# Kernel optimization log

Hardware: AMD Instinct MI355X
Metric: run time of the kernel (lower is better)

The kernel has to match this reference:

```python
import jax, jax.numpy as jnp
import numpy as np

N, L, E, NB, H = 128, 200, 128, 2, 2
ITEM = 50000
TEMP = 0.2
HD = E // H


def _ln(x, g, b, eps=1e-8):
    m = x.mean(-1, keepdims=True)
    v = ((x - m) ** 2).mean(-1, keepdims=True)
    return (x - m) / jnp.sqrt(v + eps) * g + b


def setup_inputs() -> dict:
    key = jax.random.key(0)
    ks = jax.random.split(key, 20)
    rng = np.random.default_rng(0)
    log_seqs = rng.integers(1, ITEM + 1, size=(N, L))
    lens = rng.integers(20, L + 1, size=(N,))
    log_seqs[np.arange(L)[None, :] < (L - lens[:, None])] = 0  # left padding, id 0
    pos_seqs = rng.integers(1, ITEM + 1, size=(N, L))
    neg_seqs = rng.integers(1, ITEM + 1, size=(N, L))
    item_emb = jax.random.normal(ks[0], (ITEM + 1, E), jnp.float32) * 0.02
    item_emb = item_emb.at[0].set(0.0)  # padding_idx=0
    s = 1.0 / np.sqrt(E)
    return {
        "item_emb": item_emb,
        "pos_emb": jax.random.normal(ks[1], (L + 1, E), jnp.float32) * 0.02,
        "W_asp": jax.random.normal(ks[2], (16, E, E), jnp.float32) * s,
        "w_weight": jax.random.normal(ks[3], (2 * E,), jnp.float32) * (1.0 / np.sqrt(2 * E)),
        "w_bias": jnp.zeros((), jnp.float32),
        "attn_ln_g": jnp.ones((NB, E), jnp.float32),
        "attn_ln_b": jnp.zeros((NB, E), jnp.float32),
        "in_proj_w": jax.random.normal(ks[4], (NB, 3 * E, E), jnp.float32) * s,
        "in_proj_b": jnp.zeros((NB, 3 * E), jnp.float32),
        "out_proj_w": jax.random.normal(ks[5], (NB, E, E), jnp.float32) * s,
        "out_proj_b": jnp.zeros((NB, E), jnp.float32),
        "fwd_ln_g": jnp.ones((NB, E), jnp.float32),
        "fwd_ln_b": jnp.zeros((NB, E), jnp.float32),
        "conv1_w": jax.random.normal(ks[6], (NB, E, E), jnp.float32) * s,
        "conv1_b": jnp.zeros((NB, E), jnp.float32),
        "conv2_w": jax.random.normal(ks[7], (NB, E, E), jnp.float32) * s,
        "conv2_b": jnp.zeros((NB, E), jnp.float32),
        "last_ln_g": jnp.ones((E,), jnp.float32),
        "last_ln_b": jnp.zeros((E,), jnp.float32),
        "user_ids": jnp.asarray(rng.integers(0, 100000, size=(N,)), jnp.int32),
        "log_seqs": jnp.asarray(log_seqs, jnp.int32),
        "pos_seqs": jnp.asarray(pos_seqs, jnp.int32),
        "neg_seqs": jnp.asarray(neg_seqs, jnp.int32),
        "epoch": 1,
    }


def reference(item_emb, pos_emb, W_asp, w_weight, w_bias, attn_ln_g, attn_ln_b,
              in_proj_w, in_proj_b, out_proj_w, out_proj_b, fwd_ln_g, fwd_ln_b,
              conv1_w, conv1_b, conv2_w, conv2_b, last_ln_g, last_ln_b,
              user_ids, log_seqs, pos_seqs, neg_seqs, epoch):
    tmask = (log_seqs == 0)                               # (N,L) True=pad
    validL = (~tmask).astype(item_emb.dtype)              # (N,L)
    seqs0 = item_emb[log_seqs] * validL[..., None]
    pos_embs = item_emb[pos_seqs] * validL[..., None]
    neg_embs = item_emb[neg_seqs] * validL[..., None]

    validE = jnp.concatenate([validL, validL[:, -1:]], 1)  # (N,L+1)
    kv_save = jnp.concatenate([seqs0, pos_embs[:, -1:, :]], 1)  # (N,L+1,E)

    def aspects(x, valid, residual):
        a = jnp.einsum('nli,aoi->nlao', x, W_asp)          # 16 expert GEMMs batched
        if residual:
            a = a + x[:, :, None, :]
            a = a / (jnp.linalg.norm(a, axis=-1, keepdims=True) + 1e-8)
        return a * valid[:, :, None, None]

    kv4 = aspects(kv_save, validE, True)                   # (N,L+1,16,E)
    temp = aspects(kv_save, validE, False)
    nvalid = validE.sum()
    cent_loss = jnp.linalg.norm(kv_save * validE[..., None] - temp.mean(2), axis=-1).sum() / nvalid

    norm_x = kv4 / (jnp.linalg.norm(kv4, axis=-1, keepdims=True) + 1e-8)
    pos_s = (norm_x * norm_x).sum(-1)                      # (N,L+1,16)
    ttl = jnp.einsum('nlae,nlbe->nlab', norm_x, norm_x)    # pairwise cosine sims
    mi = -(pos_s / TEMP - jnp.log(jnp.exp(ttl / TEMP).sum(-1)))
    ind_loss = (mi * validE[:, :, None]).sum() / nvalid

    s = kv4.sum(2)                                         # (N,L+1,E)
    q = jnp.cumsum(s, 1) - s                               # exclusive cumsum
    cnt = jnp.cumsum(validE, 1) - validE
    q = q / (16.0 * cnt + 1e-8)[..., None] * validE[..., None]

    w_q, w_a = w_weight[:E], w_weight[E:]

    def gate(qv, a4):                                      # learned softmax gating
        logits = (qv @ w_q)[:, :, None] + a4 @ w_a + w_bias
        w = jax.nn.softmax(logits, axis=2)
        return (a4 * w[..., None]).sum(2)

    re_all = gate(q, kv4)                                  # (N,L+1,E)
    re_emb = re_all[:, :L] + kv4[:, :L].mean(2)

    neg_kv4 = aspects(neg_embs, validL, True)
    q2 = q[:, 1:, :] * validL[..., None]
    neg_t = gate(q2, neg_kv4) + neg_kv4.mean(2)
    pos_t = re_all[:, 1:, :] * validL[..., None] + (kv4[:, 1:] * validL[..., None, None]).mean(2)

    seqs = re_emb * (E ** 0.5) + pos_emb[jnp.arange(L)][None]
    seqs = seqs * validL[..., None]
    causal = jnp.where(jnp.tril(jnp.ones((L, L), bool)), 0.0, -1e9)
    scale = HD ** -0.5
    for i in range(NB):
        Qn = _ln(seqs, attn_ln_g[i], attn_ln_b[i])
        qp = Qn @ in_proj_w[i][:E].T + in_proj_b[i][:E]
        kp = seqs @ in_proj_w[i][E:2 * E].T + in_proj_b[i][E:2 * E]
        vp = seqs @ in_proj_w[i][2 * E:].T + in_proj_b[i][2 * E:]
        sp = lambda x: x.reshape(N, L, H, HD).transpose(0, 2, 1, 3)
        att = jax.nn.softmax(jnp.einsum('nhqd,nhkd->nhqk', sp(qp), sp(kp)) * scale + causal, axis=-1)
        o = jnp.einsum('nhqk,nhkd->nhqd', att, sp(vp)).transpose(0, 2, 1, 3).reshape(N, L, E)
        seqs = Qn + (o @ out_proj_w[i].T + out_proj_b[i])
        seqs = _ln(seqs, fwd_ln_g[i], fwd_ln_b[i])
        h = jax.nn.relu(seqs @ conv1_w[i].T + conv1_b[i])
        seqs = (h @ conv2_w[i].T + conv2_b[i]) + seqs
        seqs = seqs * validL[..., None]
    log_feats = _ln(seqs, last_ln_g, last_ln_b)
    pos_logits = (log_feats * pos_t).sum(-1)
    neg_logits = (log_feats * neg_t).sum(-1)
    return (pos_logits, neg_logits, ind_loss, cent_loss)
```

## Files before the change

### kernel.cpp

```cpp
#include <hip/hip_runtime.h>
#include <hip/hip_bf16.h>
#include <cstddef>

typedef __attribute__((ext_vector_type(8))) short bf16x8;
typedef __attribute__((ext_vector_type(4))) float f32x4;
typedef unsigned short ushort_t;

__device__ __forceinline__ short f2bf(float f) {
    __hip_bfloat16 h = __float2bfloat16(f);
    return __builtin_bit_cast(short, h);
}
__device__ __forceinline__ float bf2f(short s) {
    unsigned u = ((unsigned)(unsigned short)s) << 16;
    return __builtin_bit_cast(float, u);
}
__device__ __forceinline__ unsigned pk2(float a, float b) {
    return (unsigned)(unsigned short)f2bf(a) | ((unsigned)(unsigned short)f2bf(b) << 16);
}

__global__ void cvt_all(const float* __restrict__ s0, const float* __restrict__ s1,
                        const float* __restrict__ s2, const float* __restrict__ s3,
                        const float* __restrict__ s4, ushort_t* __restrict__ dst) {
    const int i = blockIdx.x * 256 + threadIdx.x;
    const int mat = i >> 14;
    const int wm = i & 16383;
    const int blk = wm >> 9;
    const int t = blk >> 2, f = blk & 3;
    const int lane = (wm >> 3) & 63;
    const int j = wm & 7;
    const int g4 = lane >> 4, nn = lane & 15;
    const int o = t * 16 + nn;
    const int k = f * 32 + g4 * 8 + j;
    const int srcoff = o * 128 + k;
    const float* src; int mbase;
    if (mat < 16)      { src = s0; mbase = mat; }
    else if (mat < 22) { src = s1; mbase = mat - 16; }
    else if (mat < 24) { src = s2; mbase = mat - 22; }
    else if (mat < 26) { src = s3; mbase = mat - 24; }
    else               { src = s4; mbase = mat - 26; }
    float v = src[(size_t)mbase * 16384 + srcoff];
    if (mat < 16 && o == k) v += 1.f;
    dst[i] = (ushort_t)f2bf(v);
}

__global__ __launch_bounds__(512, 1) void aspects2_kernel(
        const float* __restrict__ item_emb,
        const int* __restrict__ log_seqs, const int* __restrict__ pos_seqs,
        const int* __restrict__ neg_seqs,
        const ushort_t* __restrict__ Wab,
        const float* __restrict__ w_weight,
        const float* __restrict__ pos_emb,
        float* __restrict__ Gout, float* __restrict__ seqs,
        float* __restrict__ validE, float* __restrict__ validL,
        float* __restrict__ pInd, float* __restrict__ pCent,
        int nLossBlocks) {
    __shared__ ushort_t rsb[32 * 2184];
    __shared__ ushort_t xsb[32 * 136];
    __shared__ ushort_t wal_b[128];
    __shared__ int sidx[32];
    __shared__ float s_red[512];
    __shared__ float s_lg[512];
    __shared__ float s_pos[512];
    __shared__ float vld[32];
    __shared__ float centw[32];
    __shared__ float miw[32];

    const int tid = threadIdx.x;
    const int row0 = blockIdx.x * 32;
    const bool losses = (int)blockIdx.x < nLossBlocks;
    const int lane = tid & 63, w = tid >> 6;
    const int g4 = lane >> 4, nn = lane & 15;

    if (tid < 32) {
        const int rg = row0 + tid;
        int si; float vl;
        if (rg < 25728) {
            const int nq = rg / 201, l = rg % 201;
            if (l < 200) { si = log_seqs[nq * 200 + l]; vl = (si != 0) ? 1.f : 0.f; }
            else { vl = (log_seqs[nq * 200 + 199] != 0) ? 1.f : 0.f; si = pos_seqs[nq * 200 + 199]; }
            validE[rg] = vl;
        } else {
            const int rr = rg - 25728;
            vl = (log_seqs[rr] != 0) ? 1.f : 0.f;
            si = neg_seqs[rr];
            validL[rr] = vl;
        }
        sidx[tid] = si;
        vld[tid] = vl;
    }
    if (tid < 128) wal_b[tid] = (ushort_t)f2bf(w_weight[128 + tid]);
    __syncthreads();

    {
        const int r = tid >> 4, c8 = (tid & 15) * 8;
        const float vl = vld[r];
        const float* px = &item_emb[(size_t)sidx[r] * 128 + c8];
        const float4 a = *(const float4*)px;
        const float4 b = *(const float4*)(px + 4);
        *(int2*)&xsb[r * 136 + c8] = make_int2(
            (int)pk2(a.x * vl, a.y * vl), (int)pk2(a.z * vl, a.w * vl));
        *(int2*)&xsb[r * 136 + c8 + 4] = make_int2(
            (int)pk2(b.x * vl, b.y * vl), (int)pk2(b.z * vl, b.w * vl));
    }
    __syncthreads();

    bf16x8 xf0[4], xf1[4], waf[4];
#pragma unroll
    for (int f = 0; f < 4; ++f) {
        xf0[f] = *(const bf16x8*)&xsb[nn * 136 + f * 32 + g4 * 8];
        xf1[f] = *(const bf16x8*)&xsb[(nn + 16) * 136 + f * 32 + g4 * 8];
        waf[f] = *(const bf16x8*)&wal_b[f * 32 + g4 * 8];
    }

    for (int al = 0; al < 2; ++al) {
        const int a = w * 2 + al;
        const ushort_t* wbase = Wab + (size_t)a * 16384 + lane * 8;
#pragma unroll
        for (int t = 0; t < 8; ++t) {
            f32x4 d0 = {0.f, 0.f, 0.f, 0.f}, d1 = d0;
#pragma unroll
            for (int f = 0; f < 4; ++f) {
                bf16x8 wf = *(const bf16x8*)&wbase[(t * 4 + f) * 512];
                d0 = __builtin_amdgcn_mfma_f32_16x16x32_bf16(wf, xf0[f], d0, 0, 0, 0);
                d1 = __builtin_amdgcn_mfma_f32_16x16x32_bf16(wf, xf1[f], d1, 0, 0, 0);
            }
            const int o0 = t * 16 + g4 * 4;
            *(int2*)&rsb[nn * 2184 + a * 136 + o0] = make_int2(
                (int)pk2(d0[0], d0[1]), (int)pk2(d0[2], d0[3]));
            *(int2*)&rsb[(nn + 16) * 2184 + a * 136 + o0] = make_int2(
                (int)pk2(d1[0], d1[1]), (int)pk2(d1[2], d1[3]));
        }
    }
    __syncthreads();

    f32x4 gram0 = {0.f,0.f,0.f,0.f}, gram1 = gram0, gram2 = gram0, gram3 = gram0;
#pragma unroll
    for (int rl = 0; rl < 4; ++rl) {
        const int row = w * 4 + rl;
        f32x4 dgr = {0.f, 0.f, 0.f, 0.f}, dlp = dgr;
#pragma unroll
        for (int f = 0; f < 4; ++f) {
            bf16x8 fr = *(const bf16x8*)&rsb[row * 2184 + nn * 136 + f * 32 + g4 * 8];
            dgr = __builtin_amdgcn_mfma_f32_16x16x32_bf16(fr, fr, dgr, 0, 0, 0);
            dlp = __builtin_amdgcn_mfma_f32_16x16x32_bf16(fr, waf[f], dlp, 0, 0, 0);
        }
        if (rl == 0) gram0 = dgr; else if (rl == 1) gram1 = dgr;
        else if (rl == 2) gram2 = dgr; else gram3 = dgr;
        if (g4 == (nn >> 2)) s_red[row * 16 + nn] = dgr[nn & 3];
        if (nn == 0) {
#pragma unroll
            for (int r = 0; r < 4; ++r) s_lg[row * 16 + g4 * 4 + r] = dlp[r];
        }
    }
    __syncthreads();

    {
        const float nrm = sqrtf(s_red[tid]);
        const float inv1 = 1.f / (nrm + 1e-8f);
        const float n2 = nrm * inv1;
        const float sg = inv1 / (n2 + 1e-8f);
        const float ts = n2 / (n2 + 1e-8f);
        const float logit = s_lg[tid] * inv1;
        float mx = logit;
#pragma unroll
        for (int m = 1; m < 16; m <<= 1) mx = fmaxf(mx, __shfl_xor(mx, m, 16));
        const float e = __expf(logit - mx);
        float ssum = e;
#pragma unroll
        for (int m = 1; m < 16; m <<= 1) ssum += __shfl_xor(ssum, m, 16);
        s_red[tid] = sg;
        s_pos[tid] = ts * ts * 5.f;
        s_lg[tid] = (e / ssum + 0.0625f) * inv1;
    }
    __syncthreads();

    {
        const int row = tid >> 4, ol = tid & 15, o8 = ol * 8;
        float g[8] = {0.f, 0.f, 0.f, 0.f, 0.f, 0.f, 0.f, 0.f};
        float sr[8] = {0.f, 0.f, 0.f, 0.f, 0.f, 0.f, 0.f, 0.f};
#pragma unroll
        for (int a = 0; a < 16; ++a) {
            const bf16x8 vb = *(const bf16x8*)&rsb[row * 2184 + a * 136 + o8];
            const float gw = s_lg[row * 16 + a];
#pragma unroll
            for (int j = 0; j < 8; ++j) {
                const float v = bf2f(vb[j]);
                g[j] += v * gw;
                if (losses) sr[j] += v;
            }
        }
        float* go = &Gout[(size_t)(row0 + row) * 128 + o8];
        *(float4*)go       = make_float4(g[0], g[1], g[2], g[3]);
        *(float4*)(go + 4) = make_float4(g[4], g[5], g[6], g[7]);
        if (losses) {
            const int rg = row0 + row;
            const int nq = rg / 201, l = rg % 201;
            if (l < 200) {
                const float4 p0 = *(const float4*)&pos_emb[l * 128 + o8];
                const float4 p1 = *(const float4*)&pos_emb[l * 128 + o8 + 4];
                const float vv = vld[row];
                float* so = &seqs[(size_t)(nq * 200 + l) * 128 + o8];
                const float SQ = 11.313708498984761f;
                *(float4*)so = make_float4((g[0] * SQ + p0.x) * vv, (g[1] * SQ + p0.y) * vv,
                                           (g[2] * SQ + p0.z) * vv, (g[3] * SQ + p0.w) * vv);
                *(float4*)(so + 4) = make_float4((g[4] * SQ + p1.x) * vv, (g[5] * SQ + p1.y) * vv,
                                                 (g[6] * SQ + p1.z) * vv, (g[7] * SQ + p1.w) * vv);
            }
            const bf16x8 xb = *(const bf16x8*)&xsb[row * 136 + o8];
            float c = 0.f;
#pragma unroll
            for (int j = 0; j < 8; ++j) {
                const float dd = 2.f * bf2f(xb[j]) - sr[j] * 0.0625f;
                c += dd * dd;
            }
            c += __shfl_xor(c, 1, 64);
            c += __shfl_xor(c, 2, 64);
            c += __shfl_xor(c, 4, 64);
            c += __shfl_xor(c, 8, 64);
            if (ol == 0) centw[row] = sqrtf(c) * vld[row];
        }
    }

    if (losses) {
#pragma unroll
        for (int rl = 0; rl < 4; ++rl) {
            const int row = w * 4 + rl;
            const f32x4 dd = (rl == 0) ? gram0 : (rl == 1) ? gram1 : (rl == 2) ? gram2 : gram3;
            const float sgb = s_red[row * 16 + nn];
            float mis = 0.f;
#pragma unroll
            for (int r = 0; r < 4; ++r) {
                const int a = g4 * 4 + r;
                const float sga = s_red[row * 16 + a];
                float eb = __expf(5.f * dd[r] * sga * sgb);
#pragma unroll
                for (int m = 1; m < 16; m <<= 1) eb += __shfl_xor(eb, m, 16);
                mis += -(s_pos[row * 16 + a] - logf(eb));
            }
            mis += __shfl_xor(mis, 16, 64);
            mis += __shfl_xor(mis, 32, 64);
            if (lane == 0) miw[row] = mis * vld[row];
        }
        __syncthreads();
        if (tid == 0) {
            float si = 0.f, sc = 0.f;
#pragma unroll
            for (int r = 0; r < 32; ++r) { si += miw[r]; sc += centw[r]; }
            pInd[blockIdx.x] = si;
            pCent[blockIdx.x] = sc;
        }
    }
}

__global__ __launch_bounds__(64) void qkv_kernel(const float* __restrict__ X,
                                                 const ushort_t* __restrict__ W3,
                                                 const float* __restrict__ b3,
                                                 const float* __restrict__ lng,
                                                 const float* __restrict__ lnb,
                                                 float* __restrict__ Xn,
                                                 ushort_t* __restrict__ qo,
                                                 ushort_t* __restrict__ ko,
                                                 ushort_t* __restrict__ vo) {
    const int lane = threadIdx.x & 63;
    const int q = lane >> 4, nn = lane & 15;
    const int m0 = blockIdx.x * 16;
    float xv[4][8];
    float s = 0.f, sq = 0.f;
    const float* xr = &X[(size_t)(m0 + nn) * 128];
#pragma unroll
    for (int f = 0; f < 4; ++f) {
        const float4 a = *(const float4*)&xr[f * 32 + q * 8];
        const float4 b = *(const float4*)&xr[f * 32 + q * 8 + 4];
        xv[f][0] = a.x; xv[f][1] = a.y; xv[f][2] = a.z; xv[f][3] = a.w;
        xv[f][4] = b.x; xv[f][5] = b.y; xv[f][6] = b.z; xv[f][7] = b.w;
        s += (a.x + a.y) + (a.z + a.w) + (b.x + b.y) + (b.z + b.w);
        sq += (a.x * a.x + a.y * a.y) + (a.z * a.z + a.w * a.w)
            + (b.x * b.x + b.y * b.y) + (b.z * b.z + b.w * b.w);
    }
    bf16x8 afr[4];
#pragma unroll
    for (int f = 0; f < 4; ++f) {
        bf16x8 v;
#pragma unroll
        for (int j = 0; j < 8; ++j) v[j] = f2bf(xv[f][j]);
        afr[f] = v;
    }
    s += __shfl_xor(s, 16, 64);  s += __shfl_xor(s, 32, 64);
    sq += __shfl_xor(sq, 16, 64); sq += __shfl_xor(sq, 32, 64);
    const float mean = s * 0.0078125f;
    const float var = fmaxf(sq * 0.0078125f - mean * mean, 0.f);
    const float inv = rsqrtf(var + 1e-8f);
    bf16x8 afq[4];
#pragma unroll
    for (int f = 0; f < 4; ++f) {
        const int c0 = f * 32 + q * 8;
        const float4 ga = *(const float4*)&lng[c0];
        const float4 gb = *(const float4*)&lng[c0 + 4];
        const float4 ba = *(const float4*)&lnb[c0];
        const float4 bb = *(const float4*)&lnb[c0 + 4];
        float y[8];
        y[0] = (xv[f][0] - mean) * inv * ga.x + ba.x;
        y[1] = (xv[f][1] - mean) * inv * ga.y + ba.y;
        y[2] = (xv[f][2] - mean) * inv * ga.z + ba.z;
        y[3] = (xv[f][3] - mean) * inv * ga.w + ba.w;
        y[4] = (xv[f][4] - mean) * inv * gb.x + bb.x;
        y[5] = (xv[f][5] - mean) * inv * gb.y + bb.y;
        y[6] = (xv[f][6] - mean) * inv * gb.z + bb.z;
        y[7] = (xv[f][7] - mean) * inv * gb.w + bb.w;
        float* xo = &Xn[(size_t)(m0 + nn) * 128 + c0];
        *(float4*)xo       = make_float4(y[0], y[1], y[2], y[3]);
        *(float4*)(xo + 4) = make_float4(y[4], y[5], y[6], y[7]);
        bf16x8 v;
#pragma unroll
        for (int j = 0; j < 8; ++j) v[j] = f2bf(y[j]);
        afq[f] = v;
    }
    ushort_t* const outs[3] = {qo, ko, vo};
#pragma unroll
    for (int mi = 0; mi < 3; ++mi) {
        const ushort_t* wbase = W3 + (size_t)mi * 16384 + lane * 8;
        f32x4 acc[8];
#pragma unroll
        for (int t = 0; t < 8; ++t) acc[t] = (f32x4){0.f, 0.f, 0.f, 0.f};
#pragma unroll
        for (int t = 0; t < 8; ++t) {
#pragma unroll
            for (int f = 0; f < 4; ++f) {
                bf16x8 b = *(const bf16x8*)&wbase[(t * 4 + f) * 512];
                acc[t] = __builtin_amdgcn_mfma_f32_16x16x32_bf16(
                    (mi == 0) ? afq[f] : afr[f], b, acc[t], 0, 0, 0);
            }
        }
        const float* bi = b3 + mi * 128;
        ushort_t* outp = outs[mi];
#pragma unroll
        for (int t = 0; t < 8; ++t) {
            const int n = t * 16 + nn;
            const float bv = bi[n];
#pragma unroll
            for (int r = 0; r < 4; ++r) {
                const int row = m0 + q * 4 + r;
                outp[(size_t)row * 128 + n] = (ushort_t)f2bf(acc[t][r] + bv);
            }
        }
    }
}

template <int LAST>
__global__ __launch_bounds__(64) void ffn_kernel(const ushort_t* __restrict__ attno,
                                                 const ushort_t* __restrict__ outWb,
                                                 const float* __restrict__ outB,
                                                 const float* __restrict__ resQn,
                                                 const float* __restrict__ lng,
                                                 const float* __restrict__ lnb,
                                                 const ushort_t* __restrict__ c1wb,
                                                 const float* __restrict__ c1b,
                                                 const ushort_t* __restrict__ c2wb,
                                                 const float* __restrict__ c2b,
                                                 const float* __restrict__ validL,
                                                 float* __restrict__ seqs,
                                                 const float* __restrict__ lastg,
                                                 const float* __restrict__ lastb,
                                                 const float* __restrict__ G,
                                                 const float* __restrict__ negt,
                                                 float* __restrict__ outp) {
    __shared__ ushort_t hls[16 * 136];
    const int lane = threadIdx.x & 63;
    const int q = lane >> 4, nn = lane & 15;
    const int m0 = blockIdx.x * 16;

    bf16x8 af[4];
    {
        const ushort_t* xb = &attno[(size_t)(m0 + nn) * 128];
#pragma unroll
        for (int f = 0; f < 4; ++f) af[f] = *(const bf16x8*)&xb[f * 32 + q * 8];
    }
    f32x4 acc[8];
#pragma unroll
    for (int t = 0; t < 8; ++t) acc[t] = (f32x4){0.f, 0.f, 0.f, 0.f};
    {
        const ushort_t* wbase = outWb + lane * 8;
#pragma unroll
        for (int t = 0; t < 8; ++t)
#pragma unroll
            for (int f = 0; f < 4; ++f) {
                bf16x8 b = *(const bf16x8*)&wbase[(t * 4 + f) * 512];
                acc[t] = __builtin_amdgcn_mfma_f32_16x16x32_bf16(af[f], b, acc[t], 0, 0, 0);
            }
    }
    float y[8][4];
    float s[4] = {0.f, 0.f, 0.f, 0.f}, sq[4] = {0.f, 0.f, 0.f, 0.f};
#pragma unroll
    for (int t = 0; t < 8; ++t) {
        const int n = t * 16 + nn;
        const float bi = outB[n];
#pragma unroll
        for (int r = 0; r < 4; ++r) {
            const float v = acc[t][r] + bi + resQn[(size_t)(m0 + q * 4 + r) * 128 + n];
            y[t][r] = v;
            s[r] += v;
            sq[r] += v * v;
        }
    }
#pragma unroll
    for (int m = 1; m < 16; m <<= 1) {
#pragma unroll
        for (int r = 0; r < 4; ++r) {
            s[r] += __shfl_xor(s[r], m, 64);
            sq[r] += __shfl_xor(sq[r], m, 64);
        }
    }
#pragma unroll
    for (int r = 0; r < 4; ++r) {
        const float mean = s[r] * 0.0078125f;
        const float var = fmaxf(sq[r] * 0.0078125f - mean * mean, 0.f);
        const float inv = rsqrtf(var + 1e-8f);
        s[r] = mean; sq[r] = inv;
    }
#pragma unroll
    for (int t = 0; t < 8; ++t) {
        const int n = t * 16 + nn;
        const float g = lng[n], b = lnb[n];
#pragma unroll
        for (int r = 0; r < 4; ++r) {
            const float v = (y[t][r] - s[r]) * sq[r] * g + b;
            y[t][r] = v;
            hls[(q * 4 + r) * 136 + n] = (ushort_t)f2bf(v);
        }
    }
    __syncthreads();
    {
        const ushort_t* xb = &hls[nn * 136];
#pragma unroll
        for (int f = 0; f < 4; ++f) af[f] = *(const bf16x8*)&xb[f * 32 + q * 8];
    }
    f32x4 acc2[8];
#pragma unroll
    for (int t = 0; t < 8; ++t) acc2[t] = (f32x4){0.f, 0.f, 0.f, 0.f};
    {
        const ushort_t* wbase = c1wb + lane * 8;
#pragma unroll
        for (int t = 0; t < 8; ++t)
#pragma unroll
            for (int f = 0; f < 4; ++f) {
                bf16x8 b = *(const bf16x8*)&wbase[(t * 4 + f) * 512];
                acc2[t] = __builtin_amdgcn_mfma_f32_16x16x32_bf16(af[f], b, acc2[t], 0, 0, 0);
            }
    }
    __syncthreads();
#pragma unroll
    for (int t = 0; t < 8; ++t) {
        const int n = t * 16 + nn;
        const float bi = c1b[n];
#pragma unroll
        for (int r = 0; r < 4; ++r)
            hls[(q * 4 + r) * 136 + n] = (ushort_t)f2bf(fmaxf(acc2[t][r] + bi, 0.f));
    }
    __syncthreads();
    {
        const ushort_t* xb = &hls[nn * 136];
#pragma unroll
        for (int f = 0; f < 4; ++f) af[f] = *(const bf16x8*)&xb[f * 32 + q * 8];
    }
    f32x4 acc3[8];
#pragma unroll
    for (int t = 0; t < 8; ++t) acc3[t] = (f32x4){0.f, 0.f, 0.f, 0.f};
    {
        const ushort_t* wbase = c2wb + lane * 8;
#pragma unroll
        for (int t = 0; t < 8; ++t)
#pragma unroll
            for (int f = 0; f < 4; ++f) {
                bf16x8 b = *(const bf16x8*)&wbase[(t * 4 + f) * 512];
                acc3[t] = __builtin_amdgcn_mfma_f32_16x16x32_bf16(af[f], b, acc3[t], 0, 0, 0);
            }
    }
    float mk[4];
#pragma unroll
    for (int r = 0; r < 4; ++r) mk[r] = validL[m0 + q * 4 + r];

    if constexpr (!LAST) {
#pragma unroll
        for (int t = 0; t < 8; ++t) {
            const int n = t * 16 + nn;
            const float bi = c2b[n];
#pragma unroll
            for (int r = 0; r < 4; ++r) {
                const int row = m0 + q * 4 + r;
                seqs[(size_t)row * 128 + n] = (acc3[t][r] + bi + y[t][r]) * mk[r];
            }
        }
    } else {
        float ov[8][4];
        float s2[4] = {0.f, 0.f, 0.f, 0.f}, q2[4] = {0.f, 0.f, 0.f, 0.f};
#pragma unroll
        for (int t = 0; t < 8; ++t) {
            const int n = t * 16 + nn;
            const float bi = c2b[n];
#pragma unroll
            for (int r = 0; r < 4; ++r) {
                const float v = (acc3[t][r] + bi + y[t][r]) * mk[r];
                ov[t][r] = v;
                s2[r] += v;
                q2[r] += v * v;
            }
        }
#pragma unroll
        for (int m = 1; m < 16; m <<= 1) {
#pragma unroll
            for (int r = 0; r < 4; ++r) {
                s2[r] += __shfl_xor(s2[r], m, 64);
                q2[r] += __shfl_xor(q2[r], m, 64);
            }
        }
#pragma unroll
        for (int r = 0; r < 4; ++r) {
            const float mean = s2[r] * 0.0078125f;
            const float var = fmaxf(q2[r] * 0.0078125f - mean * mean, 0.f);
            const float inv = rsqrtf(var + 1e-8f);
            s2[r] = mean; q2[r] = inv;
        }
        float sp[4] = {0.f, 0.f, 0.f, 0.f}, sn[4] = {0.f, 0.f, 0.f, 0.f};
        int nqr[4], lr[4];
#pragma unroll
        for (int r = 0; r < 4; ++r) {
            const int row = m0 + q * 4 + r;
            nqr[r] = row / 200;
            lr[r] = row - nqr[r] * 200;
        }
#pragma unroll
        for (int t = 0; t < 8; ++t) {
            const int n = t * 16 + nn;
            const float g = lastg[n], b = lastb[n];
#pragma unroll
            for (int r = 0; r < 4; ++r) {
                const int row = m0 + q * 4 + r;
                const float yln = (ov[t][r] - s2[r]) * q2[r] * g + b;
                sp[r] += yln * G[((size_t)nqr[r] * 201 + lr[r] + 1) * 128 + n];
                sn[r] += yln * negt[(size_t)row * 128 + n];
            }
        }
#pragma unroll
        for (int m = 1; m < 16; m <<= 1) {
#pragma unroll
            for (int r = 0; r < 4; ++r) {
                sp[r] += __shfl_xor(sp[r], m, 64);
                sn[r] += __shfl_xor(sn[r], m, 64);
            }
        }
        if (nn == 0) {
#pragma unroll
            for (int r = 0; r < 4; ++r) {
                const int row = m0 + q * 4 + r;
                outp[row] = sp[r] * mk[r];
                outp[25600 + row] = sn[r];
            }
        }
    }
}

__global__ void reduce_kernel(const float* __restrict__ pInd, const float* __restrict__ pCent,
                              int nblk, const float* __restrict__ validE, int nve,
                              float* __restrict__ outp) {
    __shared__ float a1[256], a2[256], a3[256];
    const int tid = threadIdx.x;
    float si = 0.f, sc = 0.f, nv = 0.f;
    for (int t = tid; t < nblk; t += 256) { si += pInd[t]; sc += pCent[t]; }
    for (int t = tid; t < nve; t += 256) nv += validE[t];
    a1[tid] = si; a2[tid] = sc; a3[tid] = nv;
    __syncthreads();
    for (int s = 128; s > 0; s >>= 1) {
        if (tid < s) { a1[tid] += a1[tid + s]; a2[tid] += a2[tid + s]; a3[tid] += a3[tid + s]; }
        __syncthreads();
    }
    if (tid == 0) { outp[0] = a1[0] / a3[0]; outp[1] = a2[0] / a3[0]; }
}

__global__ __launch_bounds__(256) void attn_kernel(const ushort_t* __restrict__ qp,
                                                   const ushort_t* __restrict__ kp,
                                                   const ushort_t* __restrict__ vp,
                                                   ushort_t* __restrict__ outp) {
    __shared__ ushort_t KsU[2048];
    __shared__ ushort_t VtU[2560];
    __shared__ ushort_t Pb[2560];

    const int tid = threadIdx.x, lane = tid & 63, w = tid >> 6;
    const int b = blockIdx.x;
    const int nh = b >> 2, qt = b & 3;
    const int n = nh >> 1, h = nh & 1;
    const size_t base = (size_t)n * 200 * 128 + (size_t)h * 64;
    const int qw = qt * 64 + w * 16;
    const bool wactive = qw < 200;
    const int q15 = lane & 15, g4 = lane >> 4;
    const int qglob = qw + q15;

    bf16x8 qf[2];
    {
        const int qr = (qglob < 200) ? qglob : 199;
#pragma unroll
        for (int f = 0; f < 2; ++f)
            qf[f] = *(const bf16x8*)&qp[base + (size_t)qr * 128 + f * 32 + g4 * 8];
    }
    f32x4 Oacc[4];
#pragma unroll
    for (int nt = 0; nt < 4; ++nt) Oacc[nt] = (f32x4){0.f, 0.f, 0.f, 0.f};
    float mrun = -1e30f, lrun = 0.f;

    const int kmax = min(200, qt * 64 + 64);
    ushort_t* PbW = Pb + w * 640;

    for (int jt = 0; jt < kmax; jt += 32) {
        __syncthreads();
        {
            const int k = tid >> 3, e0 = (tid & 7) * 8;
            const int krow = jt + k;
            int4 a = make_int4(0, 0, 0, 0);
            if (krow < 200) a = *(const int4*)&kp[base + (size_t)krow * 128 + e0];
            *(int4*)&KsU[(k * 128 + ((e0 * 2) ^ ((k & 7) << 4))) >> 1] = a;
        }
        {
            const int k = tid & 31, e0 = (tid >> 5) * 8;
            const int vrow = jt + k;
            int4 a = make_int4(0, 0, 0, 0);
            if (vrow < 200) a = *(const int4*)&vp[base + (size_t)vrow * 128 + e0];
            VtU[(e0 + 0) * 40 + k] = (ushort_t)((unsigned)a.x & 0xFFFF);
            VtU[(e0 + 1) * 40 + k] = (ushort_t)((unsigned)a.x >> 16);
            VtU[(e0 + 2) * 40 + k] = (ushort_t)((unsigned)a.y & 0xFFFF);
            VtU[(e0 + 3) * 40 + k] = (ushort_t)((unsigned)a.y >> 16);
            VtU[(e0 + 4) * 40 + k] = (ushort_t)((unsigned)a.z & 0xFFFF);
            VtU[(e0 + 5) * 40 + k] = (ushort_t)((unsigned)a.z >> 16);
            VtU[(e0 + 6) * 40 + k] = (ushort_t)((unsigned)a.w & 0xFFFF);
            VtU[(e0 + 7) * 40 + k] = (ushort_t)((unsigned)a.w >> 16);
        }
        __syncthreads();
        if (!wactive) continue;

        f32x4 d0 = {0.f, 0.f, 0.f, 0.f}, d1 = d0;
#pragma unroll
        for (int f = 0; f < 2; ++f) {
            const int ebyte = g4 * 16 + f * 64;
            const int sw = ebyte ^ ((q15 & 7) << 4);
            bf16x8 a0 = *(const bf16x8*)&KsU[(q15 * 128 + sw) >> 1];
            bf16x8 a1 = *(const bf16x8*)&KsU[((q15 + 16) * 128 + sw) >> 1];
            d0 = __builtin_amdgcn_mfma_f32_16x16x32_bf16(a0, qf[f], d0, 0, 0, 0);
            d1 = __builtin_amdgcn_mfma_f32_16x16x32_bf16(a1, qf[f], d1, 0, 0, 0);
        }
        const int kb = jt + g4 * 4;
        float p[8];
        float tmax = -1e30f;
#pragma unroll
        for (int r = 0; r < 4; ++r) {
            const float s0 = (kb + r      <= qglob) ? d0[r] * 0.125f : -1e30f;
            const float s1 = (kb + r + 16 <= qglob) ? d1[r] * 0.125f : -1e30f;
            p[r] = s0; p[r + 4] = s1;
            tmax = fmaxf(tmax, fmaxf(s0, s1));
        }
        tmax = fmaxf(tmax, __shfl_xor(tmax, 16, 64));
        tmax = fmaxf(tmax, __shfl_xor(tmax, 32, 64));
        const float mnew = fmaxf(mrun, tmax);
        const float corr = __expf(mrun - mnew);
        mrun = mnew;
        float tsum = 0.f;
#pragma unroll
        for (int i = 0; i < 8; ++i) {
            float pe = __expf(p[i] - mnew);
            pe = bf2f(f2bf(pe));
            p[i] = pe;
            tsum += pe;
        }
        tsum += __shfl_xor(tsum, 16, 64);
        tsum += __shfl_xor(tsum, 32, 64);
        lrun = lrun * corr + tsum;
        const int kl = g4 * 4;
        *(unsigned*)&PbW[q15 * 40 + kl]          = pk2(p[0], p[1]);
        *(unsigned*)&PbW[q15 * 40 + kl + 2]      = pk2(p[2], p[3]);
        *(unsigned*)&PbW[q15 * 40 + 16 + kl]     = pk2(p[4], p[5]);
        *(unsigned*)&PbW[q15 * 40 + 16 + kl + 2] = pk2(p[6], p[7]);
        asm volatile("" ::: "memory");
        float corr_r[4];
#pragma unroll
        for (int r = 0; r < 4; ++r) corr_r[r] = __shfl(corr, g4 * 4 + r, 64);
#pragma unroll
        for (int nt = 0; nt < 4; ++nt) {
#pragma unroll
            for (int r = 0; r < 4; ++r) Oacc[nt][r] *= corr_r[r];
        }
        bf16x8 pa = *(const bf16x8*)&PbW[q15 * 40 + g4 * 8];
#pragma unroll
        for (int nt = 0; nt < 4; ++nt) {
            bf16x8 vb = *(const bf16x8*)&VtU[(nt * 16 + q15) * 40 + g4 * 8];
            Oacc[nt] = __builtin_amdgcn_mfma_f32_16x16x32_bf16(pa, vb, Oacc[nt], 0, 0, 0);
        }
    }
    if (wactive) {
        float linv[4];
#pragma unroll
        for (int r = 0; r < 4; ++r) linv[r] = 1.f / __shfl(lrun, g4 * 4 + r, 64);
#pragma unroll
        for (int r = 0; r < 4; ++r) {
            const int qg = qw + g4 * 4 + r;
            if (qg < 200) {
#pragma unroll
                for (int nt = 0; nt < 4; ++nt)
                    outp[base + (size_t)qg * 128 + nt * 16 + q15] =
                        (ushort_t)f2bf(Oacc[nt][r] * linv[r]);
            }
        }
    }
}

extern "C" void kernel_launch(void* const* d_in, const int* in_sizes, int n_in,
                              void* d_out, int out_size, void* d_ws, size_t ws_size,
                              hipStream_t stream) {
    (void)in_sizes; (void)n_in; (void)out_size; (void)ws_size;
    const float* item_emb = (const float*)d_in[0];
    const float* pos_emb  = (const float*)d_in[1];
    const float* W_asp    = (const float*)d_in[2];
    const float* w_weight = (const float*)d_in[3];
    const float* attn_g = (const float*)d_in[5];
    const float* attn_b = (const float*)d_in[6];
    const float* inW    = (const float*)d_in[7];
    const float* inB    = (const float*)d_in[8];
    const float* outW   = (const float*)d_in[9];
    const float* outB   = (const float*)d_in[10];
    const float* fwd_g  = (const float*)d_in[11];
    const float* fwd_b  = (const float*)d_in[12];
    const float* c1w    = (const float*)d_in[13];
    const float* c1b    = (const float*)d_in[14];
    const float* c2w    = (const float*)d_in[15];
    const float* c2b    = (const float*)d_in[16];
    const float* last_g = (const float*)d_in[17];
    const float* last_b = (const float*)d_in[18];
    const int* log_seqs = (const int*)d_in[20];
    const int* pos_seqs = (const int*)d_in[21];
    const int* neg_seqs = (const int*)d_in[22];

    float* ws = (float*)d_ws;
    const size_t S = (size_t)128 * 201 * 128;
    ushort_t* qp = (ushort_t*)ws;
    ushort_t* kp = qp + (size_t)25600 * 128;
    float* G     = ws + 2 * S;
    float* negt  = ws + 3 * S;
    float* seqs  = ws + 4 * S;
    float* Qn    = ws + 5 * S;
    ushort_t* vp    = (ushort_t*)(ws + 6 * S);
    ushort_t* attno = (ushort_t*)(ws + 7 * S);
    ushort_t* wb  = (ushort_t*)(ws + 8 * S);
    ushort_t* Wab  = wb;
    ushort_t* inWb = Wab + 262144;
    ushort_t* outWb = inWb + 98304;
    ushort_t* c1b_w = outWb + 32768;
    ushort_t* c2b_w = c1b_w + 32768;
    float* validE = ws + 8 * S + 229376;
    float* validL = validE + 128 * 201;
    float* pInd   = validL + 128 * 200;
    float* pCent  = pInd + 804;
    float* outF   = (float*)d_out;

    cvt_all<<<dim3(1792), dim3(256), 0, stream>>>(W_asp, inW, outW, c1w, c2w, wb);
    aspects2_kernel<<<dim3(1604), dim3(512), 0, stream>>>(
        item_emb, log_seqs, pos_seqs, neg_seqs, Wab, w_weight, pos_emb,
        G, seqs, validE, validL, pInd, pCent, 804);
    reduce_kernel<<<dim3(1), dim3(256), 0, stream>>>(
        pInd, pCent, 804, validE, 128 * 201, outF + 51200);

    for (int i = 0; i < 2; ++i) {
        qkv_kernel<<<dim3(1600), dim3(64), 0, stream>>>(
            seqs, inWb + (size_t)i * 3 * 16384, inB + (size_t)i * 384,
            attn_g + i * 128, attn_b + i * 128, Qn, qp, kp, vp);
        attn_kernel<<<dim3(1024), dim3(256), 0, stream>>>(qp, kp, vp, attno);
        if (i == 0) {
            ffn_kernel<0><<<dim3(1600), dim3(64), 0, stream>>>(
                attno, outWb + (size_t)i * 16384, outB + i * 128, Qn,
                fwd_g + i * 128, fwd_b + i * 128,
                c1b_w + (size_t)i * 16384, c1b + i * 128,
                c2b_w + (size_t)i * 16384, c2b + i * 128,
                validL, seqs, nullptr, nullptr, nullptr, nullptr, nullptr);
        } else {
            ffn_kernel<1><<<dim3(1600), dim3(64), 0, stream>>>(
                attno, outWb + (size_t)i * 16384, outB + i * 128, Qn,
                fwd_g + i * 128, fwd_b + i * 128,
                c1b_w + (size_t)i * 16384, c1b + i * 128,
                c2b_w + (size_t)i * 16384, c2b + i * 128,
                validL, nullptr, last_g, last_b, G, negt, outF);
        }
    }
}
```

Before: 201.6 us.

## Halve aspects kernel rows per block to allow two blocks per CU

Changes the aspects kernel from 32 to 16 rows per block, which halves the shared-memory buffers and doubles the grid. Launch bounds now ask for two blocks per CU, so more work can be resident at once to hide latency. The epilogue is remapped so each thread handles 4 columns instead of 8, and the loss partials and reduce launch are sized for twice as many blocks. In exchange, each block reuses each loaded W_asp fragment across only one 16-row MFMA tile instead of two, so weight reads from cache double.

Result: slower. 232.5 us (+15.3%).

```diff
diff --git a/kernel.cpp b/kernel.cpp
--- a/kernel.cpp
+++ b/kernel.cpp
@@ -43,7 +43,7 @@
     dst[i] = (ushort_t)f2bf(v);
 }
 
-__global__ __launch_bounds__(512, 1) void aspects2_kernel(
+__global__ __launch_bounds__(512, 2) void aspects2_kernel(
         const float* __restrict__ item_emb,
         const int* __restrict__ log_seqs, const int* __restrict__ pos_seqs,
         const int* __restrict__ neg_seqs,
@@ -54,24 +54,24 @@
         float* __restrict__ validE, float* __restrict__ validL,
         float* __restrict__ pInd, float* __restrict__ pCent,
         int nLossBlocks) {
-    __shared__ ushort_t rsb[32 * 2184];
-    __shared__ ushort_t xsb[32 * 136];
+    __shared__ ushort_t rsb[16 * 2184];
+    __shared__ ushort_t xsb[16 * 136];
     __shared__ ushort_t wal_b[128];
-    __shared__ int sidx[32];
-    __shared__ float s_red[512];
-    __shared__ float s_lg[512];
-    __shared__ float s_pos[512];
-    __shared__ float vld[32];
-    __shared__ float centw[32];
-    __shared__ float miw[32];
+    __shared__ int sidx[16];
+    __shared__ float s_red[256];
+    __shared__ float s_lg[256];
+    __shared__ float s_pos[256];
+    __shared__ float vld[16];
+    __shared__ float centw[16];
+    __shared__ float miw[16];
 
     const int tid = threadIdx.x;
-    const int row0 = blockIdx.x * 32;
+    const int row0 = blockIdx.x * 16;
     const bool losses = (int)blockIdx.x < nLossBlocks;
     const int lane = tid & 63, w = tid >> 6;
     const int g4 = lane >> 4, nn = lane & 15;
 
-    if (tid < 32) {
+    if (tid < 16) {
         const int rg = row0 + tid;
         int si; float vl;
         if (rg < 25728) {
@@ -91,7 +91,7 @@
     if (tid < 128) wal_b[tid] = (ushort_t)f2bf(w_weight[128 + tid]);
     __syncthreads();
 
-    {
+    if (tid < 256) {
         const int r = tid >> 4, c8 = (tid & 15) * 8;
         const float vl = vld[r];
         const float* px = &item_emb[(size_t)sidx[r] * 128 + c8];
@@ -104,11 +104,10 @@
     }
     __syncthreads();
 
-    bf16x8 xf0[4], xf1[4], waf[4];
+    bf16x8 xf[4], waf[4];
 #pragma unroll
     for (int f = 0; f < 4; ++f) {
-        xf0[f] = *(const bf16x8*)&xsb[nn * 136 + f * 32 + g4 * 8];
-        xf1[f] = *(const bf16x8*)&xsb[(nn + 16) * 136 + f * 32 + g4 * 8];
+        xf[f] = *(const bf16x8*)&xsb[nn * 136 + f * 32 + g4 * 8];
         waf[f] = *(const bf16x8*)&wal_b[f * 32 + g4 * 8];
     }
 
@@ -117,26 +116,23 @@
         const ushort_t* wbase = Wab + (size_t)a * 16384 + lane * 8;
 #pragma unroll
         for (int t = 0; t < 8; ++t) {
-            f32x4 d0 = {0.f, 0.f, 0.f, 0.f}, d1 = d0;
+            f32x4 d0 = {0.f, 0.f, 0.f, 0.f};
 #pragma unroll
             for (int f = 0; f < 4; ++f) {
                 bf16x8 wf = *(const bf16x8*)&wbase[(t * 4 + f) * 512];
-                d0 = __builtin_amdgcn_mfma_f32_16x16x32_bf16(wf, xf0[f], d0, 0, 0, 0);
-                d1 = __builtin_amdgcn_mfma_f32_16x16x32_bf16(wf, xf1[f], d1, 0, 0, 0);
+                d0 = __builtin_amdgcn_mfma_f32_16x16x32_bf16(wf, xf[f], d0, 0, 0, 0);
             }
             const int o0 = t * 16 + g4 * 4;
             *(int2*)&rsb[nn * 2184 + a * 136 + o0] = make_int2(
                 (int)pk2(d0[0], d0[1]), (int)pk2(d0[2], d0[3]));
-            *(int2*)&rsb[(nn + 16) * 2184 + a * 136 + o0] = make_int2(
-                (int)pk2(d1[0], d1[1]), (int)pk2(d1[2], d1[3]));
-        }
-    }
-    __syncthreads();
-
-    f32x4 gram0 = {0.f,0.f,0.f,0.f}, gram1 = gram0, gram2 = gram0, gram3 = gram0;
-#pragma unroll
-    for (int rl = 0; rl < 4; ++rl) {
-        const int row = w * 4 + rl;
+        }
+    }
+    __syncthreads();
+
+    f32x4 gram0 = {0.f,0.f,0.f,0.f}, gram1 = gram0;
+#pragma unroll
+    for (int rl = 0; rl < 2; ++rl) {
+        const int row = w * 2 + rl;
         f32x4 dgr = {0.f, 0.f, 0.f, 0.f}, dlp = dgr;
 #pragma unroll
         for (int f = 0; f < 4; ++f) {
@@ -144,8 +140,7 @@
             dgr = __builtin_amdgcn_mfma_f32_16x16x32_bf16(fr, fr, dgr, 0, 0, 0);
             dlp = __builtin_amdgcn_mfma_f32_16x16x32_bf16(fr, waf[f], dlp, 0, 0, 0);
         }
-        if (rl == 0) gram0 = dgr; else if (rl == 1) gram1 = dgr;
-        else if (rl == 2) gram2 = dgr; else gram3 = dgr;
+        if (rl == 0) gram0 = dgr; else gram1 = dgr;
         if (g4 == (nn >> 2)) s_red[row * 16 + nn] = dgr[nn & 3];
         if (nn == 0) {
 #pragma unroll
@@ -154,7 +149,7 @@
     }
     __syncthreads();
 
-    {
+    if (tid < 256) {
         const float nrm = sqrtf(s_red[tid]);
         const float inv1 = 1.f / (nrm + 1e-8f);
         const float n2 = nrm * inv1;
@@ -175,57 +170,53 @@
     __syncthreads();
 
     {
-        const int row = tid >> 4, ol = tid & 15, o8 = ol * 8;
-        float g[8] = {0.f, 0.f, 0.f, 0.f, 0.f, 0.f, 0.f, 0.f};
-        float sr[8] = {0.f, 0.f, 0.f, 0.f, 0.f, 0.f, 0.f, 0.f};
+        const int row = tid >> 5, ol = tid & 31, o4 = ol * 4;
+        float g[4] = {0.f, 0.f, 0.f, 0.f};
+        float sr[4] = {0.f, 0.f, 0.f, 0.f};
 #pragma unroll
         for (int a = 0; a < 16; ++a) {
-            const bf16x8 vb = *(const bf16x8*)&rsb[row * 2184 + a * 136 + o8];
+            const int2 pk = *(const int2*)&rsb[row * 2184 + a * 136 + o4];
+            const float v0 = __builtin_bit_cast(float, ((unsigned)pk.x) << 16);
+            const float v1 = __builtin_bit_cast(float, ((unsigned)pk.x) & 0xFFFF0000u);
+            const float v2 = __builtin_bit_cast(float, ((unsigned)pk.y) << 16);
+            const float v3 = __builtin_bit_cast(float, ((unsigned)pk.y) & 0xFFFF0000u);
             const float gw = s_lg[row * 16 + a];
-#pragma unroll
-            for (int j = 0; j < 8; ++j) {
-                const float v = bf2f(vb[j]);
-                g[j] += v * gw;
-                if (losses) sr[j] += v;
-            }
-        }
-        float* go = &Gout[(size_t)(row0 + row) * 128 + o8];
-        *(float4*)go       = make_float4(g[0], g[1], g[2], g[3]);
-        *(float4*)(go + 4) = make_float4(g[4], g[5], g[6], g[7]);
+            g[0] += v0 * gw; g[1] += v1 * gw; g[2] += v2 * gw; g[3] += v3 * gw;
+            if (losses) { sr[0] += v0; sr[1] += v1; sr[2] += v2; sr[3] += v3; }
+        }
+        *(float4*)&Gout[(size_t)(row0 + row) * 128 + o4] = make_float4(g[0], g[1], g[2], g[3]);
         if (losses) {
             const int rg = row0 + row;
             const int nq = rg / 201, l = rg % 201;
             if (l < 200) {
-                const float4 p0 = *(const float4*)&pos_emb[l * 128 + o8];
-                const float4 p1 = *(const float4*)&pos_emb[l * 128 + o8 + 4];
+                const float4 p0 = *(const float4*)&pos_emb[l * 128 + o4];
                 const float vv = vld[row];
-                float* so = &seqs[(size_t)(nq * 200 + l) * 128 + o8];
+                float* so = &seqs[(size_t)(nq * 200 + l) * 128 + o4];
                 const float SQ = 11.313708498984761f;
                 *(float4*)so = make_float4((g[0] * SQ + p0.x) * vv, (g[1] * SQ + p0.y) * vv,
                                            (g[2] * SQ + p0.z) * vv, (g[3] * SQ + p0.w) * vv);
-                *(float4*)(so + 4) = make_float4((g[4] * SQ + p1.x) * vv, (g[5] * SQ + p1.y) * vv,
-                                                 (g[6] * SQ + p1.z) * vv, (g[7] * SQ + p1.w) * vv);
-            }
-            const bf16x8 xb = *(const bf16x8*)&xsb[row * 136 + o8];
-            float c = 0.f;
-#pragma unroll
-            for (int j = 0; j < 8; ++j) {
-                const float dd = 2.f * bf2f(xb[j]) - sr[j] * 0.0625f;
-                c += dd * dd;
-            }
-            c += __shfl_xor(c, 1, 64);
-            c += __shfl_xor(c, 2, 64);
-            c += __shfl_xor(c, 4, 64);
-            c += __shfl_xor(c, 8, 64);
+            }
+            const int2 xk = *(const int2*)&xsb[row * 136 + o4];
+            const float x0 = __builtin_bit_cast(float, ((unsigned)xk.x) << 16);
+            const float x1 = __builtin_bit_cast(float, ((unsigned)xk.x) & 0xFFFF0000u);
+            const float x2 = __builtin_bit_cast(float, ((unsigned)xk.y) << 16);
+            const float x3 = __builtin_bit_cast(float, ((unsigned)xk.y) & 0xFFFF0000u);
+            const float d0 = 2.f * x0 - sr[0] * 0.0625f;
+            const float d1 = 2.f * x1 - sr[1] * 0.0625f;
+            const float d2 = 2.f * x2 - sr[2] * 0.0625f;
+            const float d3 = 2.f * x3 - sr[3] * 0.0625f;
+            float c = d0 * d0 + d1 * d1 + d2 * d2 + d3 * d3;
+#pragma unroll
+            for (int m = 1; m < 32; m <<= 1) c += __shfl_xor(c, m, 64);
             if (ol == 0) centw[row] = sqrtf(c) * vld[row];
         }
     }
 
     if (losses) {
 #pragma unroll
-        for (int rl = 0; rl < 4; ++rl) {
-            const int row = w * 4 + rl;
-            const f32x4 dd = (rl == 0) ? gram0 : (rl == 1) ? gram1 : (rl == 2) ? gram2 : gram3;
+        for (int rl = 0; rl < 2; ++rl) {
+            const int row = w * 2 + rl;
+            const f32x4 dd = (rl == 0) ? gram0 : gram1;
             const float sgb = s_red[row * 16 + nn];
             float mis = 0.f;
 #pragma unroll
@@ -245,7 +236,7 @@
         if (tid == 0) {
             float si = 0.f, sc = 0.f;
 #pragma unroll
-            for (int r = 0; r < 32; ++r) { si += miw[r]; sc += centw[r]; }
+            for (int r = 0; r < 16; ++r) { si += miw[r]; sc += centw[r]; }
             pInd[blockIdx.x] = si;
             pCent[blockIdx.x] = sc;
         }
@@ -754,15 +745,15 @@
     float* validE = ws + 8 * S + 229376;
     float* validL = validE + 128 * 201;
     float* pInd   = validL + 128 * 200;
-    float* pCent  = pInd + 804;
+    float* pCent  = pInd + 1608;
     float* outF   = (float*)d_out;
 
     cvt_all<<<dim3(1792), dim3(256), 0, stream>>>(W_asp, inW, outW, c1w, c2w, wb);
-    aspects2_kernel<<<dim3(1604), dim3(512), 0, stream>>>(
+    aspects2_kernel<<<dim3(3208), dim3(512), 0, stream>>>(
         item_emb, log_seqs, pos_seqs, neg_seqs, Wab, w_weight, pos_emb,
-        G, seqs, validE, validL, pInd, pCent, 804);
+        G, seqs, validE, validL, pInd, pCent, 1608);
     reduce_kernel<<<dim3(1), dim3(256), 0, stream>>>(
-        pInd, pCent, 804, validE, 128 * 201, outF + 51200);
+        pInd, pCent, 1608, validE, 128 * 201, outF + 51200);
 
     for (int i = 0; i < 2; ++i) {
         qkv_kernel<<<dim3(1600), dim3(64), 0, stream>>>(
```
